# Kernel tuning notes

Hardware: AMD Instinct MI355X
Metric: run time of the kernel (lower is better)

The kernel has to match this reference:

```python
import jax, jax.numpy as jnp
import numpy as np

B, N, H, D = 4, 16384, 8, 128
KERNEL_SIZE, STRIDE = 32, 16


def setup_inputs() -> dict:
    key = jax.random.key(0)
    k1, k2, k3 = jax.random.split(key, 3)
    x = jax.random.normal(k1, (B, N, H, D), dtype=jnp.float32)
    weight = jax.random.normal(k2, (KERNEL_SIZE,), dtype=jnp.float32)
    pe = jax.random.normal(k3, (KERNEL_SIZE, D), dtype=jnp.float32)
    return {"x": x, "weight": weight, "pe": pe}


def reference(x, weight, pe):
    # y[b,m,h,d] = sum_k (x[b, m*stride + k, h, d] + pe[k,d]) * w[k] / kernel_size
    Bx, Nx, Hx, Dx = x.shape
    K = weight.shape[0]
    M = (Nx - K) // STRIDE + 1  # num_blocks
    # window gather indices [M, K]
    idx = jnp.arange(M)[:, None] * STRIDE + jnp.arange(K)[None, :]
    xw = x[:, idx]  # [B, M, K, H, D]
    # split the pe term out: sum_k pe[k]*w[k] is a constant [D] vector
    y = jnp.einsum('bmkhd,k->bmhd', xw, weight) + jnp.einsum('kd,k->d', pe, weight)
    return (y / K).astype(x.dtype)
```

## Files before the change

kernel.cpp:

```cpp
#include <hip/hip_runtime.h>

#define Bc 4
#define Nc 16384
#define Hc 8
#define Dc 128
#define Kc 32
#define STRIDEc 16
#define Mc 1023

__global__ __launch_bounds__(256) void compress_kv_kernel(
    const float* __restrict__ x,
    const float* __restrict__ w,
    const float* __restrict__ pe,
    float* __restrict__ out)
{
    __shared__ float s_w[Kc];
    __shared__ __align__(16) float s_bias[Dc];

    const int tid = threadIdx.x;

    if (tid < Kc) s_w[tid] = w[tid] * (1.0f / (float)Kc);
    __syncthreads();

    if (tid < Dc) {
        float b = 0.0f;
        #pragma unroll 8
        for (int k = 0; k < Kc; ++k) b += pe[k * Dc + tid] * s_w[k];
        s_bias[tid] = b;
    }
    __syncthreads();

    const int bm = blockIdx.x;
    const int m  = bm % Mc;
    const int b  = bm / Mc;
    const int d4 = tid & 31;
    const int h  = tid >> 5;

    const float4* __restrict__ x4 = (const float4*)x;

    int base = ((b * Nc + m * STRIDEc) * Hc + h) * (Dc / 4) + d4;
    const int step = Hc * (Dc / 4);

    float4 acc = ((const float4*)s_bias)[d4];

    #pragma unroll 8
    for (int k = 0; k < Kc; ++k) {
        float4 xv = x4[base + k * step];
        float wk = s_w[k];
        acc.x += xv.x * wk;
        acc.y += xv.y * wk;
        acc.z += xv.z * wk;
        acc.w += xv.w * wk;
    }

    float4* __restrict__ out4 = (float4*)out;
    const int obase = ((b * Mc + m) * Hc + h) * (Dc / 4) + d4;
    out4[obase] = acc;
}

extern "C" void kernel_launch(void* const* d_in, const int* in_sizes, int n_in,
                              void* d_out, int out_size, void* d_ws, size_t ws_size,
                              hipStream_t stream) {
    const float* x  = (const float*)d_in[0];
    const float* w  = (const float*)d_in[1];
    const float* pe = (const float*)d_in[2];
    float* out = (float*)d_out;

    const int grid = Bc * Mc;
    compress_kv_kernel<<<grid, 256, 0, stream>>>(x, w, pe, out);
}
```

Measured before the change: 371.4 us.

## Tile 8 overlapping windows per block to reuse each input row twice

Each block now computes 8 consecutive output windows, loading the 144 shared input rows once and applying each row to both overlapping windows with the matching weight half. This removes the duplicate global reads caused by stride being half the kernel size, and it amortizes the per-block weight and bias setup. The trade-offs are a grid roughly 8x smaller, which lowers occupancy, and higher register pressure from 8 float4 accumulators and heavy unrolling.

Result: slower. 381.2 us (+2.6%).

```diff
diff --git a/kernel.cpp b/kernel.cpp
--- a/kernel.cpp
+++ b/kernel.cpp
@@ -7,6 +7,7 @@
 #define Kc 32
 #define STRIDEc 16
 #define Mc 1023
+#define Tm 8
 
 __global__ __launch_bounds__(256) void compress_kv_kernel(
     const float* __restrict__ x,
@@ -23,39 +24,81 @@
     __syncthreads();
 
     if (tid < Dc) {
-        float b = 0.0f;
-        #pragma unroll 8
-        for (int k = 0; k < Kc; ++k) b += pe[k * Dc + tid] * s_w[k];
-        s_bias[tid] = b;
+        float bsum = 0.0f;
+        #pragma unroll
+        for (int k = 0; k < Kc; ++k) bsum += pe[k * Dc + tid] * s_w[k];
+        s_bias[tid] = bsum;
     }
     __syncthreads();
 
-    const int bm = blockIdx.x;
-    const int m  = bm % Mc;
-    const int b  = bm / Mc;
-    const int d4 = tid & 31;
-    const int h  = tid >> 5;
+    const int NT  = (Mc + Tm - 1) / Tm;
+    const int b   = blockIdx.x / NT;
+    const int m0  = (blockIdx.x % NT) * Tm;
+    const int n0  = m0 * STRIDEc;
+    const int d4  = tid & 31;
+    const int h   = tid >> 5;
 
     const float4* __restrict__ x4 = (const float4*)x;
+    const int step = Hc * (Dc / 4);
+    const int base = ((b * Nc + n0) * Hc + h) * (Dc / 4) + d4;
 
-    int base = ((b * Nc + m * STRIDEc) * Hc + h) * (Dc / 4) + d4;
-    const int step = Hc * (Dc / 4);
+    const float4 bias = ((const float4*)s_bias)[d4];
+    float4 acc[Tm];
+    #pragma unroll
+    for (int j = 0; j < Tm; ++j) acc[j] = bias;
 
-    float4 acc = ((const float4*)s_bias)[d4];
+    const int windows = (Mc - m0 < Tm) ? (Mc - m0) : Tm;
 
-    #pragma unroll 8
-    for (int k = 0; k < Kc; ++k) {
-        float4 xv = x4[base + k * step];
-        float wk = s_w[k];
-        acc.x += xv.x * wk;
-        acc.y += xv.y * wk;
-        acc.z += xv.z * wk;
-        acc.w += xv.w * wk;
+    if (windows == Tm && n0 + 16 * Tm + 16 <= Nc) {
+        #pragma unroll
+        for (int i = 0; i <= Tm; ++i) {
+            #pragma unroll
+            for (int t = 0; t < 16; ++t) {
+                const float4 xv = x4[base + (16 * i + t) * step];
+                if (i < Tm) {
+                    const float wk = s_w[t];
+                    acc[i].x += xv.x * wk; acc[i].y += xv.y * wk;
+                    acc[i].z += xv.z * wk; acc[i].w += xv.w * wk;
+                }
+                if (i >= 1) {
+                    const float wk = s_w[16 + t];
+                    acc[i-1].x += xv.x * wk; acc[i-1].y += xv.y * wk;
+                    acc[i-1].z += xv.z * wk; acc[i-1].w += xv.w * wk;
+                }
+            }
+        }
+    } else {
+        const int rows = (Nc - n0 < 16 * Tm + 16) ? (Nc - n0) : (16 * Tm + 16);
+        #pragma unroll
+        for (int i = 0; i <= Tm; ++i) {
+            #pragma unroll
+            for (int t = 0; t < 16; ++t) {
+                const int r = 16 * i + t;
+                if (r < rows) {
+                    const float4 xv = x4[base + r * step];
+                    if (i < windows) {
+                        const float wk = s_w[t];
+                        acc[i].x += xv.x * wk; acc[i].y += xv.y * wk;
+                        acc[i].z += xv.z * wk; acc[i].w += xv.w * wk;
+                    }
+                    if (i >= 1 && (i - 1) < windows) {
+                        const float wk = s_w[16 + t];
+                        acc[i-1].x += xv.x * wk; acc[i-1].y += xv.y * wk;
+                        acc[i-1].z += xv.z * wk; acc[i-1].w += xv.w * wk;
+                    }
+                }
+            }
+        }
     }
 
     float4* __restrict__ out4 = (float4*)out;
-    const int obase = ((b * Mc + m) * Hc + h) * (Dc / 4) + d4;
-    out4[obase] = acc;
+    #pragma unroll
+    for (int j = 0; j < Tm; ++j) {
+        if (j < windows) {
+            const int obase = ((b * Mc + (m0 + j)) * Hc + h) * (Dc / 4) + d4;
+            out4[obase] = acc[j];
+        }
+    }
 }
 
 extern "C" void kernel_launch(void* const* d_in, const int* in_sizes, int n_in,
@@ -66,6 +109,7 @@
     const float* pe = (const float*)d_in[2];
     float* out = (float*)d_out;
 
-    const int grid = Bc * Mc;
+    const int NT = (Mc + Tm - 1) / Tm;
+    const int grid = Bc * NT;
     compress_kv_kernel<<<grid, 256, 0, stream>>>(x, w, pe, out);
 }
```
